# Kernel tuning notes

Hardware: AMD Instinct MI355X
Metric: run time of the kernel (lower is better)

Reference implementation:

```python
import jax, jax.numpy as jnp
import numpy as np

TAU = 2.0          # LIF membrane time constant (spikingjelly default)
V_TH = 1.0         # v_threshold
V_RESET = 0.0      # hard reset value
ATAN_ALPHA = 2.0   # surrogate.ATan default alpha
EPS = 1e-12        # F.normalize eps

@jax.custom_vjp
def spike_fn(x):
    # Heaviside forward, ATan surrogate backward
    return (x >= 0).astype(x.dtype)

def _spike_fwd(x):
    return spike_fn(x), x

def _spike_bwd(x, g):
    sg = (ATAN_ALPHA / 2.0) / (1.0 + (jnp.pi / 2.0 * ATAN_ALPHA * x) ** 2)
    return (g * sg,)

spike_fn.defvjp(_spike_fwd, _spike_bwd)

def setup_inputs() -> dict:
    key = jax.random.key(0)
    k1, k2 = jax.random.split(key)
    T, B, F, H = 32, 512, 2048, 2048
    x_seq = jax.random.normal(k1, (T, B, F), dtype=jnp.float32)
    lim = float(np.sqrt(6.0 / (F + H)))  # xavier_uniform
    W = jax.random.uniform(k2, (H, F), dtype=jnp.float32, minval=-lim, maxval=lim)
    b = jnp.zeros((H,), dtype=jnp.float32)
    return {"x_seq": x_seq, "W": W, "b": b}

def reference(x_seq, W, b):
    # Linear: [T,B,F] @ [F,H] -> [T,B,H]
    cur = jnp.einsum('tbf,hf->tbh', x_seq, W) + b
    # F.normalize(dim=-1): L2 normalize the injected current per neuron vector
    norm = jnp.maximum(jnp.sqrt(jnp.sum(cur * cur, axis=-1, keepdims=True)), EPS)
    cur = cur / norm

    def step(v, c):
        # LIF charge: v <- v + (x - (v - v_reset)) / tau
        v = v + (c - (v - V_RESET)) / TAU
        s = spike_fn(v - V_TH)
        sd = jax.lax.stop_gradient(s)  # detach_reset=True
        v = v * (1.0 - sd) + V_RESET * sd  # hard reset
        return v, s

    v0 = jnp.zeros(cur.shape[1:], dtype=cur.dtype)  # [B,H]
    _, spk_seq = jax.lax.scan(step, v0, cur)  # spk_seq: [T,B,H]
    count = spk_seq.sum(axis=0)  # [B,H]
    return spk_seq, count
```

## Files before the change

### kernel.cpp

```cpp
#include <hip/hip_runtime.h>
#include <hip/hip_bf16.h>

#define T_SZ 32
#define B_SZ 512
#define F_SZ 2048
#define H_SZ 2048
#define M_SZ (T_SZ * B_SZ)

#define BM 128
#define BN 256
#define BK 64

typedef int   i32x8  __attribute__((ext_vector_type(8)));
typedef float f32x16 __attribute__((ext_vector_type(16)));
typedef unsigned short u16x8 __attribute__((ext_vector_type(8)));

__device__ __forceinline__ void gload_lds16(const void* g, void* l) {
    __builtin_amdgcn_global_load_lds(
        (const __attribute__((address_space(1))) unsigned int*)g,
        (__attribute__((address_space(3))) unsigned int*)l,
        16, 0, 0);
}

__device__ __forceinline__ float bf16_bits_to_f32(unsigned short u) {
    return __uint_as_float(((unsigned)u) << 16);
}

__global__ __launch_bounds__(256) void cvt_fp8_kernel(const float* __restrict__ in,
                                                      unsigned int* __restrict__ out,
                                                      float scale, int n8) {
    int i = blockIdx.x * 256 + threadIdx.x;
    if (i >= n8) return;
    float4 v0 = ((const float4*)in)[2 * i];
    float4 v1 = ((const float4*)in)[2 * i + 1];
    int w0 = __builtin_amdgcn_cvt_pk_fp8_f32(v0.x * scale, v0.y * scale, 0, false);
    w0     = __builtin_amdgcn_cvt_pk_fp8_f32(v0.z * scale, v0.w * scale, w0, true);
    int w1 = __builtin_amdgcn_cvt_pk_fp8_f32(v1.x * scale, v1.y * scale, 0, false);
    w1     = __builtin_amdgcn_cvt_pk_fp8_f32(v1.z * scale, v1.w * scale, w1, true);
    ((uint2*)out)[i] = make_uint2((unsigned)w0, (unsigned)w1);
}

__global__ __launch_bounds__(256) void gemm_fp8_kernel(const unsigned char* __restrict__ A,
                                                       const unsigned char* __restrict__ Bt,
                                                       const float* __restrict__ bias,
                                                       __hip_bfloat16* __restrict__ C)
{
    __shared__ __align__(16) unsigned char As[BM * BK];
    __shared__ __align__(16) unsigned char Bs[BN * BK];

    const int tid  = threadIdx.x;
    const int lane = tid & 63;
    const int wave = tid >> 6;
    const int wm   = wave >> 1;
    const int wn   = wave & 1;
    const int m0   = blockIdx.y * BM;
    const int n0   = blockIdx.x * BN;
    const int l31  = lane & 31;
    const int kh   = lane >> 5;

    f32x16 acc[2][4] = {};

    for (int k0 = 0; k0 < F_SZ; k0 += BK) {
        __syncthreads();
        #pragma unroll
        for (int j = 0; j < 2; ++j) {
            int c   = j * 256 + tid;
            int row = c >> 2;
            int u   = (c & 3) ^ ((row >> 1) & 3);
            gload_lds16(A + (size_t)(m0 + row) * F_SZ + k0 + u * 16, (void*)(As + c * 16));
        }
        #pragma unroll
        for (int j = 0; j < 4; ++j) {
            int c   = j * 256 + tid;
            int row = c >> 2;
            int u   = (c & 3) ^ ((row >> 1) & 3);
            gload_lds16(Bt + (size_t)(n0 + row) * F_SZ + k0 + u * 16, (void*)(Bs + c * 16));
        }
        __syncthreads();

        i32x8 af[2], bq[4];
        #pragma unroll
        for (int i = 0; i < 2; ++i) {
            const int ra = wm * 64 + i * 32 + l31;
            const int sa = (ra >> 1) & 3;
            ((int4*)&af[i])[0] = *(const int4*)(As + ra * 64 + (((kh * 2 + 0) ^ sa) * 16));
            ((int4*)&af[i])[1] = *(const int4*)(As + ra * 64 + (((kh * 2 + 1) ^ sa) * 16));
        }
        #pragma unroll
        for (int i = 0; i < 4; ++i) {
            const int rb = wn * 128 + i * 32 + l31;
            const int sb = (rb >> 1) & 3;
            ((int4*)&bq[i])[0] = *(const int4*)(Bs + rb * 64 + (((kh * 2 + 0) ^ sb) * 16));
            ((int4*)&bq[i])[1] = *(const int4*)(Bs + rb * 64 + (((kh * 2 + 1) ^ sb) * 16));
        }
        #pragma unroll
        for (int mi = 0; mi < 2; ++mi)
            #pragma unroll
            for (int ni = 0; ni < 4; ++ni)
                acc[mi][ni] = __builtin_amdgcn_mfma_scale_f32_32x32x64_f8f6f4(
                    af[mi], bq[ni], acc[mi][ni],
                    0 , 0 ,
                    0, 0x7f7f7f7f,
                    0, 0x7f7f7f7f);
    }

    #pragma unroll
    for (int ni = 0; ni < 4; ++ni) {
        const int gn = n0 + wn * 128 + ni * 32 + l31;
        const float bv = bias[gn];
        #pragma unroll
        for (int mi = 0; mi < 2; ++mi) {
            const int gmb = m0 + wm * 64 + mi * 32 + 4 * kh;
            #pragma unroll
            for (int r = 0; r < 16; ++r) {
                const int grow = gmb + (r & 3) + 8 * (r >> 2);
                C[(size_t)grow * H_SZ + gn] = __float2bfloat16(acc[mi][ni][r] * (1.0f / 256.0f) + bv);
            }
        }
    }
}

__global__ __launch_bounds__(256) void row_ss_kernel(const __hip_bfloat16* __restrict__ cur,
                                                     float* __restrict__ ninv) {
    const int lane = threadIdx.x & 63;
    const int row  = blockIdx.x * 4 + (threadIdx.x >> 6);
    const __hip_bfloat16* rp = cur + (size_t)row * H_SZ;

    float s = 0.f;
    #pragma unroll
    for (int i = 0; i < 4; ++i) {
        const u16x8 pk = *(const u16x8*)(rp + i * 512 + lane * 8);
        #pragma unroll
        for (int j = 0; j < 8; ++j) {
            float f = bf16_bits_to_f32(pk[j]);
            s += f * f;
        }
    }
    #pragma unroll
    for (int off = 32; off >= 1; off >>= 1) s += __shfl_down(s, off, 64);
    if (lane == 0) ninv[row] = 1.0f / fmaxf(sqrtf(s), 1e-12f);
}

__global__ __launch_bounds__(256) void lif_scan_kernel(const __hip_bfloat16* __restrict__ cur,
                                                       const float* __restrict__ ninv,
                                                       float* __restrict__ spk,
                                                       float* __restrict__ cnt)
{
    const int gid = blockIdx.x * 256 + threadIdx.x;
    const int b   = gid >> 9;
    const int h0  = (gid & 511) * 4;

    float v[4]  = {0, 0, 0, 0};
    float cn[4] = {0, 0, 0, 0};
    #pragma unroll
    for (int t = 0; t < T_SZ; ++t) {
        const size_t off = (size_t)(t * B_SZ + b) * H_SZ + h0;
        const ushort4 pk = *(const ushort4*)(cur + off);
        const float inv  = ninv[t * B_SZ + b];
        float so[4];
        {
            float c;
            c = bf16_bits_to_f32(pk.x) * inv; v[0] += (c - v[0]) * 0.5f;
            c = bf16_bits_to_f32(pk.y) * inv; v[1] += (c - v[1]) * 0.5f;
            c = bf16_bits_to_f32(pk.z) * inv; v[2] += (c - v[2]) * 0.5f;
            c = bf16_bits_to_f32(pk.w) * inv; v[3] += (c - v[3]) * 0.5f;
        }
        #pragma unroll
        for (int j = 0; j < 4; ++j) {
            float s = (v[j] >= 1.0f) ? 1.0f : 0.0f;
            so[j] = s;
            cn[j] += s;
            v[j] = (s != 0.f) ? 0.f : v[j];
        }
        *(float4*)(spk + off) = make_float4(so[0], so[1], so[2], so[3]);
    }
    *(float4*)(cnt + (size_t)b * H_SZ + h0) = make_float4(cn[0], cn[1], cn[2], cn[3]);
}

extern "C" void kernel_launch(void* const* d_in, const int* in_sizes, int n_in,
                              void* d_out, int out_size, void* d_ws, size_t ws_size,
                              hipStream_t stream) {
    const float* x    = (const float*)d_in[0];
    const float* W    = (const float*)d_in[1];
    const float* bias = (const float*)d_in[2];

    float* spk = (float*)d_out;
    float* cnt = spk + (size_t)T_SZ * B_SZ * H_SZ;

    char* ws = (char*)d_ws;
    unsigned char* x8    = (unsigned char*)ws;
    unsigned char* W8    = x8 + (size_t)M_SZ * F_SZ;
    __hip_bfloat16* curb = (__hip_bfloat16*)(W8 + (size_t)H_SZ * F_SZ);
    float* ninv          = (float*)((char*)curb + (size_t)M_SZ * H_SZ * 2);

    cvt_fp8_kernel<<<(M_SZ * F_SZ / 8) / 256, 256, 0, stream>>>(x, (unsigned int*)x8, 1.0f,   M_SZ * F_SZ / 8);
    cvt_fp8_kernel<<<(H_SZ * F_SZ / 8) / 256, 256, 0, stream>>>(W, (unsigned int*)W8, 256.0f, H_SZ * F_SZ / 8);
    gemm_fp8_kernel<<<dim3(H_SZ / BN, M_SZ / BM), 256, 0, stream>>>(x8, W8, bias, curb);
    row_ss_kernel<<<M_SZ / 4, 256, 0, stream>>>(curb, ninv);
    lif_scan_kernel<<<(B_SZ * H_SZ / 4) / 256, 256, 0, stream>>>(curb, ninv, spk, cnt);
}
```

Measured before the change: 410.2 us.

## Fuse row sum-of-squares into GEMM epilogue and retile to 128x128x128

Removes the separate row_ss kernel. The GEMM epilogue now computes per-row partial sums of squares, reduces them across lanes with shuffles, and accumulates them into a zeroed buffer with atomics. The LIF scan derives the inverse norm from that buffer. The GEMM tile also changes from 128x256x64 to 128x128x128 with an 8-way XOR swizzle, two k-substeps and a launch_bounds occupancy hint. This avoids a full re-read of the bf16 current tensor, at the cost of atomics, an extra init kernel, a sum of squares taken from fp32 values rather than from the bf16-rounded ones, and a smaller N tile with less reuse.

```diff
diff --git a/kernel.cpp b/kernel.cpp
--- a/kernel.cpp
+++ b/kernel.cpp
@@ -8,8 +8,8 @@
 #define M_SZ (T_SZ * B_SZ)
 
 #define BM 128
-#define BN 256
-#define BK 64
+#define BN 128
+#define BK 128
 
 typedef int   i32x8  __attribute__((ext_vector_type(8)));
 typedef float f32x16 __attribute__((ext_vector_type(16)));
@@ -40,10 +40,15 @@
     ((uint2*)out)[i] = make_uint2((unsigned)w0, (unsigned)w1);
 }
 
-__global__ __launch_bounds__(256) void gemm_fp8_kernel(const unsigned char* __restrict__ A,
-                                                       const unsigned char* __restrict__ Bt,
-                                                       const float* __restrict__ bias,
-                                                       __hip_bfloat16* __restrict__ C)
+__global__ __launch_bounds__(256) void init_ss_kernel(float4* __restrict__ ss4) {
+    ss4[blockIdx.x * 256 + threadIdx.x] = make_float4(0.f, 0.f, 0.f, 0.f);
+}
+
+__global__ __launch_bounds__(256, 3) void gemm_fp8_kernel(const unsigned char* __restrict__ A,
+                                                          const unsigned char* __restrict__ Bt,
+                                                          const float* __restrict__ bias,
+                                                          __hip_bfloat16* __restrict__ C,
+                                                          float* __restrict__ ss)
 {
     __shared__ __align__(16) unsigned char As[BM * BK];
     __shared__ __align__(16) unsigned char Bs[BN * BK];
@@ -58,55 +63,55 @@
     const int l31  = lane & 31;
     const int kh   = lane >> 5;
 
-    f32x16 acc[2][4] = {};
+    f32x16 acc[2][2] = {};
 
     for (int k0 = 0; k0 < F_SZ; k0 += BK) {
         __syncthreads();
         #pragma unroll
-        for (int j = 0; j < 2; ++j) {
-            int c   = j * 256 + tid;
-            int row = c >> 2;
-            int u   = (c & 3) ^ ((row >> 1) & 3);
-            gload_lds16(A + (size_t)(m0 + row) * F_SZ + k0 + u * 16, (void*)(As + c * 16));
-        }
-        #pragma unroll
         for (int j = 0; j < 4; ++j) {
             int c   = j * 256 + tid;
-            int row = c >> 2;
-            int u   = (c & 3) ^ ((row >> 1) & 3);
+            int row = c >> 3;
+            int u   = (c & 7) ^ (row & 7);
+            gload_lds16(A + (size_t)(m0 + row) * F_SZ + k0 + u * 16, (void*)(As + c * 16));
+        }
+        #pragma unroll
+        for (int j = 0; j < 4; ++j) {
+            int c   = j * 256 + tid;
+            int row = c >> 3;
+            int u   = (c & 7) ^ (row & 7);
             gload_lds16(Bt + (size_t)(n0 + row) * F_SZ + k0 + u * 16, (void*)(Bs + c * 16));
         }
         __syncthreads();
 
-        i32x8 af[2], bq[4];
-        #pragma unroll
-        for (int i = 0; i < 2; ++i) {
-            const int ra = wm * 64 + i * 32 + l31;
-            const int sa = (ra >> 1) & 3;
-            ((int4*)&af[i])[0] = *(const int4*)(As + ra * 64 + (((kh * 2 + 0) ^ sa) * 16));
-            ((int4*)&af[i])[1] = *(const int4*)(As + ra * 64 + (((kh * 2 + 1) ^ sa) * 16));
-        }
-        #pragma unroll
-        for (int i = 0; i < 4; ++i) {
-            const int rb = wn * 128 + i * 32 + l31;
-            const int sb = (rb >> 1) & 3;
-            ((int4*)&bq[i])[0] = *(const int4*)(Bs + rb * 64 + (((kh * 2 + 0) ^ sb) * 16));
-            ((int4*)&bq[i])[1] = *(const int4*)(Bs + rb * 64 + (((kh * 2 + 1) ^ sb) * 16));
-        }
-        #pragma unroll
-        for (int mi = 0; mi < 2; ++mi)
+        #pragma unroll
+        for (int s = 0; s < 2; ++s) {
+            i32x8 af[2], bq[2];
             #pragma unroll
-            for (int ni = 0; ni < 4; ++ni)
-                acc[mi][ni] = __builtin_amdgcn_mfma_scale_f32_32x32x64_f8f6f4(
-                    af[mi], bq[ni], acc[mi][ni],
-                    0 , 0 ,
-                    0, 0x7f7f7f7f,
-                    0, 0x7f7f7f7f);
-    }
-
+            for (int i = 0; i < 2; ++i) {
+                const int ra = wm * 64 + i * 32 + l31;
+                const int rb = wn * 64 + i * 32 + l31;
+                const int ua = s * 4 + kh * 2;
+                ((int4*)&af[i])[0] = *(const int4*)(As + ra * BK + (((ua + 0) ^ (ra & 7)) * 16));
+                ((int4*)&af[i])[1] = *(const int4*)(As + ra * BK + (((ua + 1) ^ (ra & 7)) * 16));
+                ((int4*)&bq[i])[0] = *(const int4*)(Bs + rb * BK + (((ua + 0) ^ (rb & 7)) * 16));
+                ((int4*)&bq[i])[1] = *(const int4*)(Bs + rb * BK + (((ua + 1) ^ (rb & 7)) * 16));
+            }
+            #pragma unroll
+            for (int mi = 0; mi < 2; ++mi)
+                #pragma unroll
+                for (int ni = 0; ni < 2; ++ni)
+                    acc[mi][ni] = __builtin_amdgcn_mfma_scale_f32_32x32x64_f8f6f4(
+                        af[mi], bq[ni], acc[mi][ni],
+                        0 , 0 ,
+                        0, 0x7f7f7f7f,
+                        0, 0x7f7f7f7f);
+        }
+    }
+
+    float ssl[2][16];
     #pragma unroll
-    for (int ni = 0; ni < 4; ++ni) {
-        const int gn = n0 + wn * 128 + ni * 32 + l31;
+    for (int ni = 0; ni < 2; ++ni) {
+        const int gn = n0 + wn * 64 + ni * 32 + l31;
         const float bv = bias[gn];
         #pragma unroll
         for (int mi = 0; mi < 2; ++mi) {
@@ -114,35 +119,32 @@
             #pragma unroll
             for (int r = 0; r < 16; ++r) {
                 const int grow = gmb + (r & 3) + 8 * (r >> 2);
-                C[(size_t)grow * H_SZ + gn] = __float2bfloat16(acc[mi][ni][r] * (1.0f / 256.0f) + bv);
+                const float val = acc[mi][ni][r] * (1.0f / 256.0f) + bv;
+                C[(size_t)grow * H_SZ + gn] = __float2bfloat16(val);
+                if (ni == 0) ssl[mi][r] = val * val;
+                else         ssl[mi][r] += val * val;
             }
         }
     }
-}
-
-__global__ __launch_bounds__(256) void row_ss_kernel(const __hip_bfloat16* __restrict__ cur,
-                                                     float* __restrict__ ninv) {
-    const int lane = threadIdx.x & 63;
-    const int row  = blockIdx.x * 4 + (threadIdx.x >> 6);
-    const __hip_bfloat16* rp = cur + (size_t)row * H_SZ;
-
-    float s = 0.f;
     #pragma unroll
-    for (int i = 0; i < 4; ++i) {
-        const u16x8 pk = *(const u16x8*)(rp + i * 512 + lane * 8);
-        #pragma unroll
-        for (int j = 0; j < 8; ++j) {
-            float f = bf16_bits_to_f32(pk[j]);
-            s += f * f;
-        }
-    }
-    #pragma unroll
-    for (int off = 32; off >= 1; off >>= 1) s += __shfl_down(s, off, 64);
-    if (lane == 0) ninv[row] = 1.0f / fmaxf(sqrtf(s), 1e-12f);
+    for (int mi = 0; mi < 2; ++mi) {
+        const int gmb = m0 + wm * 64 + mi * 32 + 4 * kh;
+        #pragma unroll
+        for (int r = 0; r < 16; ++r) {
+            float p = ssl[mi][r];
+            p += __shfl_xor(p, 1, 64);
+            p += __shfl_xor(p, 2, 64);
+            p += __shfl_xor(p, 4, 64);
+            p += __shfl_xor(p, 8, 64);
+            p += __shfl_xor(p, 16, 64);
+            if (l31 == 0)
+                atomicAdd(ss + gmb + (r & 3) + 8 * (r >> 2), p);
+        }
+    }
 }
 
 __global__ __launch_bounds__(256) void lif_scan_kernel(const __hip_bfloat16* __restrict__ cur,
-                                                       const float* __restrict__ ninv,
+                                                       const float* __restrict__ ss,
                                                        float* __restrict__ spk,
                                                        float* __restrict__ cnt)
 {
@@ -156,7 +158,7 @@
     for (int t = 0; t < T_SZ; ++t) {
         const size_t off = (size_t)(t * B_SZ + b) * H_SZ + h0;
         const ushort4 pk = *(const ushort4*)(cur + off);
-        const float inv  = ninv[t * B_SZ + b];
+        const float inv  = 1.0f / fmaxf(sqrtf(ss[t * B_SZ + b]), 1e-12f);
         float so[4];
         {
             float c;
@@ -191,11 +193,11 @@
     unsigned char* x8    = (unsigned char*)ws;
     unsigned char* W8    = x8 + (size_t)M_SZ * F_SZ;
     __hip_bfloat16* curb = (__hip_bfloat16*)(W8 + (size_t)H_SZ * F_SZ);
-    float* ninv          = (float*)((char*)curb + (size_t)M_SZ * H_SZ * 2);
-
+    float* ss            = (float*)((char*)curb + (size_t)M_SZ * H_SZ * 2);
+
+    init_ss_kernel<<<M_SZ / 1024, 256, 0, stream>>>((float4*)ss);
     cvt_fp8_kernel<<<(M_SZ * F_SZ / 8) / 256, 256, 0, stream>>>(x, (unsigned int*)x8, 1.0f,   M_SZ * F_SZ / 8);
     cvt_fp8_kernel<<<(H_SZ * F_SZ / 8) / 256, 256, 0, stream>>>(W, (unsigned int*)W8, 256.0f, H_SZ * F_SZ / 8);
-    gemm_fp8_kernel<<<dim3(H_SZ / BN, M_SZ / BM), 256, 0, stream>>>(x8, W8, bias, curb);
-    row_ss_kernel<<<M_SZ / 4, 256, 0, stream>>>(curb, ninv);
-    lif_scan_kernel<<<(B_SZ * H_SZ / 4) / 256, 256, 0, stream>>>(curb, ninv, spk, cnt);
-}
+    gemm_fp8_kernel<<<dim3(H_SZ / BN, M_SZ / BM), 256, 0, stream>>>(x8, W8, bias, curb, ss);
+    lif_scan_kernel<<<(B_SZ * H_SZ / 4) / 256, 256, 0, stream>>>(curb, ss, spk, cnt);
+}
```

Measured after the change: 355.2 us, median of 2. -13.4%, faster.
